# Kernel tuning notes

Hardware: AMD Instinct MI355X
Metric: run time of the kernel (lower is better)

## Reference

```python
import jax, jax.numpy as jnp
import numpy as np

B, S, D = 4, 2048, 1024


def setup_inputs() -> dict:
    key = jax.random.key(0)
    kq, k1, k2, k3 = jax.random.split(key, 4)
    w_scale = 1.0 / np.sqrt(D)  # ~ glorot scale for square Dense
    q = jax.random.normal(kq, (B, S, D), dtype=jnp.float32)
    Wq = jax.random.normal(k1, (D, D), dtype=jnp.float32) * w_scale
    Wk = jax.random.normal(k2, (D, D), dtype=jnp.float32) * w_scale  # unused in self-attn path (bug in original)
    Wv = jax.random.normal(k3, (D, D), dtype=jnp.float32) * w_scale
    # causal mask: 1 = masked (future), matching tf.where(mask == 1, -1e9, scores)
    mask = jnp.triu(jnp.ones((S, S), dtype=jnp.int32), k=1)
    return {"q": q, "Wq": Wq, "Wk": Wk, "Wv": Wv, "mask": mask}


def reference(q, Wq, Wk, Wv, mask):
    # Self-attention path of the original: k=None, v=None.
    WQ = jnp.einsum('bsd,de->bse', q, Wq)
    # Faithful to the original code: dense_v is applied for BOTH K and V.
    WKV = jnp.einsum('bsd,de->bse', q, Wv)
    d_k = jnp.asarray(D, dtype=q.dtype)
    scores = jnp.einsum('bqd,bkd->bqk', WQ, WKV) / jnp.sqrt(d_k)  # [B,S,S]
    scores = jnp.where(mask == 1, jnp.asarray(-1e9, scores.dtype), scores)
    attn = jax.nn.softmax(scores, axis=-1)
    return jnp.einsum('bqk,bkd->bqd', attn, WKV)
```

## Files before the change

### kernel.cpp

```cpp
#include <hip/hip_runtime.h>


typedef unsigned short u16;
typedef short short8 __attribute__((ext_vector_type(8)));
typedef float floatx4 __attribute__((ext_vector_type(4)));

#define S_LEN 2048
#define D_DIM 1024
#define BK 64

__device__ inline u16 f2b(float f) {
  unsigned u = __float_as_uint(f);
  return (u16)((u + 0x7fffu + ((u >> 16) & 1u)) >> 16);
}

__device__ __forceinline__ void gload16(const u16* g, u16* l) {
  __builtin_amdgcn_global_load_lds(
      (const __attribute__((address_space(1))) void*)g,
      (__attribute__((address_space(3))) void*)l, 16, 0, 0);
}

__global__ __launch_bounds__(256)
void prep(const float* __restrict__ q, u16* __restrict__ qb16,
          const float* __restrict__ Wq, u16* __restrict__ Wqt,
          const float* __restrict__ Wv, u16* __restrict__ Wvt,
          float* __restrict__ rowsum) {
  int id = blockIdx.x, tid = threadIdx.x;
  if (id < 4096) {
    if (id < 4) {
      int o = id * 2048 + tid * 8;
      float4 zz = {0.f, 0.f, 0.f, 0.f};
      *(float4*)&rowsum[o] = zz;
      *(float4*)&rowsum[o + 4] = zz;
    }
    size_t idx = ((size_t)id * 256 + tid) * 8;
    float4 a0 = *(const float4*)&q[idx];
    float4 a1 = *(const float4*)&q[idx + 4];
    short8 v;
    v[0] = (short)f2b(a0.x); v[1] = (short)f2b(a0.y);
    v[2] = (short)f2b(a0.z); v[3] = (short)f2b(a0.w);
    v[4] = (short)f2b(a1.x); v[5] = (short)f2b(a1.y);
    v[6] = (short)f2b(a1.z); v[7] = (short)f2b(a1.w);
    *(short8*)&qb16[idx] = v;
    return;
  }
  __shared__ u16 tile[64][65];
  int id2 = id - 4096;
  int z = id2 >> 8;
  int idx4 = id2 & 255;
  int c0 = (idx4 & 15) * 64, r0 = (idx4 >> 4) * 64;
  const float* src = z ? Wv : Wq;
  u16* dst = z ? Wvt : Wqt;
  int tx = tid & 63, ty = tid >> 6;
#pragma unroll
  for (int i = 0; i < 16; ++i)
    tile[i * 4 + ty][tx] =
        f2b(src[(size_t)(r0 + i * 4 + ty) * 1024 + (c0 + tx)]);
  __syncthreads();
#pragma unroll
  for (int i = 0; i < 16; ++i)
    dst[(size_t)(c0 + i * 4 + ty) * 1024 + (r0 + tx)] = tile[tx][i * 4 + ty];
}

__global__ __launch_bounds__(512, 2)
void gemm_proj(const u16* __restrict__ A, const u16* __restrict__ B0,
               const u16* __restrict__ B1, u16* __restrict__ C0,
               u16* __restrict__ C1, u16* __restrict__ WKVt) {
  __shared__ __align__(16) u16 lds[65536];

  int id = blockIdx.x;
  int xcd = id & 7, i5 = id >> 3;
  int m_idx = xcd * 4 + (i5 & 3);
  int n_idx = i5 >> 2;
  int z = n_idx >> 2;
  int n0 = (n_idx & 3) * 256;
  int m0 = m_idx * 256;
  const u16* Bp = z ? B1 : B0;
  u16* Cp = z ? C1 : C0;

  int tid = threadIdx.x;
  int wv = tid >> 6, lane = tid & 63, quad = lane >> 4, l15 = lane & 15;
  int wm = wv >> 2, wn = wv & 3;

  int off_g[2];
#pragma unroll
  for (int l = 0; l < 2; ++l) {
    int chunk = (wv * 2 + l) * 64 + lane;
    int r = chunk >> 3, cs = chunk & 7;
    off_g[l] = r * 1024 + (cs ^ (r & 7)) * 8;
  }
  const u16* As0 = A + (size_t)m0 * 1024;
  const u16* As1 = A + (size_t)(m0 + 128) * 1024;
  const u16* Bs0 = Bp + (size_t)n0 * 1024;
  const u16* Bs1 = Bp + (size_t)(n0 + 128) * 1024;

#define PSTAGE(src, reg)                                                     \
  {                                                                          \
    _Pragma("unroll") for (int l = 0; l < 2; ++l)                            \
        gload16((src) + off_g[l], &lds[(reg) * 8192 + (wv * 2 + l) * 512]);  \
  }

  int aoff[2], boff[2];
#pragma unroll
  for (int kk = 0; kk < 2; ++kk) {
    int c = ((kk * 4 + quad) ^ (l15 & 7)) * 8;
    aoff[kk] = l15 * 64 + c;
    boff[kk] = ((wn & 1) * 64 + l15) * 64 + c;
  }
  const u16* A0p = &lds[(0 + wm) * 8192];
  const u16* A1p = &lds[(4 + wm) * 8192];
  const u16* B0p = &lds[(2 + (wn >> 1)) * 8192];
  const u16* B1p = &lds[(6 + (wn >> 1)) * 8192];

  floatx4 acc[8][4];
#pragma unroll
  for (int i = 0; i < 8; ++i)
#pragma unroll
    for (int j = 0; j < 4; ++j) acc[i][j] = (floatx4){0.f, 0.f, 0.f, 0.f};

#define BARp() __builtin_amdgcn_s_barrier()
#define WLG() asm volatile("s_waitcnt lgkmcnt(0)" ::: "memory")
#define WVM(n) asm volatile("s_waitcnt vmcnt(" #n ")" ::: "memory")

#define RDA(dst, base, fb)                                                 \
  _Pragma("unroll") for (int f = 0; f < 4; ++f)                            \
  _Pragma("unroll") for (int kk = 0; kk < 2; ++kk)                         \
      dst[f][kk] = *(const short8*)&(base)[((fb) + f) * 1024 + aoff[kk]];
#define RDB(dst, base, fb)                                                 \
  _Pragma("unroll") for (int f = 0; f < 2; ++f)                            \
  _Pragma("unroll") for (int kk = 0; kk < 2; ++kk)                         \
      dst[f][kk] = *(const short8*)&(base)[((fb) + f) * 1024 + boff[kk]];
#define MMQ(mh, nh, afq, bfq)                                              \
  __builtin_amdgcn_s_setprio(1);                                           \
  _Pragma("unroll") for (int f = 0; f < 4; ++f)                            \
  _Pragma("unroll") for (int g2 = 0; g2 < 2; ++g2)                         \
  _Pragma("unroll") for (int kk = 0; kk < 2; ++kk)                         \
      acc[(mh) * 4 + f][(nh) * 2 + g2] =                                   \
          __builtin_amdgcn_mfma_f32_16x16x32_bf16(                         \
              afq[f][kk], bfq[g2][kk], acc[(mh) * 4 + f][(nh) * 2 + g2],   \
              0, 0, 0);                                                    \
  __builtin_amdgcn_s_setprio(0);

  PSTAGE(As0, 0); PSTAGE(As1, 1); PSTAGE(Bs0, 2); PSTAGE(Bs1, 3);
  PSTAGE(As0 + 64, 4); PSTAGE(As1 + 64, 5); PSTAGE(Bs0 + 64, 6);
  PSTAGE(Bs1 + 64, 7);
  WVM(8);
  BARp();

#pragma unroll 1
  for (int it = 0; it < 8; ++it) {
    int kb2 = it * 128 + 128, kb3 = it * 128 + 192;
    short8 af[4][2], bf0[2][2], bf1[2][2];
    RDA(af, A0p, 0); RDB(bf0, B0p, 0);
    BARp(); WLG();
    MMQ(0, 0, af, bf0);
    BARp();
    RDB(bf1, B0p, 2);
    BARp(); WLG();
    MMQ(0, 1, af, bf1);
    BARp();
    RDA(af, A0p, 4);
    if (it < 7) PSTAGE(Bs0 + kb2, 2);
    BARp(); WLG();
    MMQ(1, 1, af, bf1);
    BARp();
    if (it < 7) { PSTAGE(Bs1 + kb2, 3); PSTAGE(As0 + kb2, 0); }
    BARp();
    MMQ(1, 0, af, bf0);
    if (it < 7) { WVM(6); } else { WVM(0); }
    BARp();
    RDA(af, A1p, 0); RDB(bf0, B1p, 0);
    if (it < 7) PSTAGE(As1 + kb2, 1);
    BARp(); WLG();
    MMQ(0, 0, af, bf0);
    BARp();
    RDB(bf1, B1p, 2);
    BARp(); WLG();
    MMQ(0, 1, af, bf1);
    BARp();
    RDA(af, A1p, 4);
    if (it < 7) PSTAGE(Bs0 + kb3, 6);
    BARp(); WLG();
    MMQ(1, 1, af, bf1);
    BARp();
    if (it < 7) {
      PSTAGE(Bs1 + kb3, 7); PSTAGE(As0 + kb3, 4); PSTAGE(As1 + kb3, 5);
    }
    BARp();
    MMQ(1, 0, af, bf0);
    if (it < 7) WVM(8);
    BARp();
  }

  asm volatile("s_waitcnt vmcnt(0) lgkmcnt(0)" ::: "memory");
#pragma unroll
  for (int mf = 0; mf < 8; ++mf)
#pragma unroll
    for (int nf = 0; nf < 4; ++nf)
#pragma unroll
      for (int r = 0; r < 4; ++r)
        Cp[(size_t)(m0 + wm * 128 + mf * 16 + quad * 4 + r) * D_DIM +
           (n0 + wn * 64 + nf * 16 + l15)] = f2b(acc[mf][nf][r]);

  if (z) {
    int b = m0 >> 11, srow = m0 & 2047;
    u16* Wt = WKVt + (size_t)b * D_DIM * S_LEN;
#pragma unroll
    for (int ph = 0; ph < 2; ++ph) {
      BARp();
      if ((wn >> 1) == ph) {
#pragma unroll
        for (int mf = 0; mf < 8; ++mf)
#pragma unroll
          for (int nf = 0; nf < 4; ++nf)
#pragma unroll
            for (int r = 0; r < 4; ++r)
              lds[((wn & 1) * 64 + nf * 16 + l15) * 272 +
                  (wm * 128 + mf * 16 + quad * 4 + r)] = f2b(acc[mf][nf][r]);
      }
      BARp();
#pragma unroll
      for (int rr = 0; rr < 8; ++rr) {
        int idx = rr * 512 + tid;
        int dl = idx >> 5, sc = idx & 31;
        *(short8*)&Wt[(size_t)(n0 + ph * 128 + dl) * S_LEN + srow + sc * 8] =
            *(const short8*)&lds[dl * 272 + sc * 8];
      }
    }
  }
}

#define GEMM64_PROLOG()                                                       \
  __shared__ __align__(16) u16 Als[2][64 * BK];                               \
  __shared__ __align__(16) u16 Bls[2][128 * BK];                              \
  int tid = threadIdx.x;                                                      \
  int wave = tid >> 6, lane = tid & 63, quad = lane >> 4, l15 = lane & 15;    \
  int wr = (wave >> 1) * 32, wc = (wave & 1) * 64;                            \
  int arow = lane >> 3;                                                       \
  int acol = ((lane & 7) ^ (arow & 7)) << 3;                                  \
  floatx4 acc[2][4];                                                          \
  _Pragma("unroll") for (int i = 0; i < 2; ++i)                               \
  _Pragma("unroll") for (int j = 0; j < 4; ++j)                               \
      acc[i][j] = (floatx4){0.f, 0.f, 0.f, 0.f};

#define GEMM64_STAGE(buf, Aptr, lda, Bptr, ldb, kb)                           \
  {                                                                           \
    _Pragma("unroll") for (int p = 0; p < 2; ++p) {                           \
      int r0 = wave * 16 + p * 8;                                             \
      gload16(&(Aptr)[(size_t)(m0 + r0 + arow) * (lda) + (kb) + acol],        \
              &Als[buf][r0 * BK]);                                            \
    }                                                                         \
    _Pragma("unroll") for (int p = 0; p < 4; ++p) {                           \
      int r0 = wave * 32 + p * 8;                                             \
      gload16(&(Bptr)[(size_t)(n0 + r0 + arow) * (ldb) + (kb) + acol],        \
              &Bls[buf][r0 * BK]);                                            \
    }                                                                         \
  }

#define GEMM64_COMP(buf)                                                      \
  {                                                                           \
    const u16* Ab = &Als[buf][0];                                             \
    const u16* Bb = &Bls[buf][0];                                             \
    _Pragma("unroll") for (int kk8 = 0; kk8 < 8; kk8 += 4) {                  \
      int cg = (((kk8 + quad) & 7) ^ (l15 & 7)) << 3;                         \
      short8 af[2], bfr[4];                                                   \
      _Pragma("unroll") for (int i = 0; i < 2; ++i)                           \
          af[i] = *(const short8*)&Ab[(wr + i * 16 + l15) * BK + cg];         \
      _Pragma("unroll") for (int j = 0; j < 4; ++j)                           \
          bfr[j] = *(const short8*)&Bb[(wc + j * 16 + l15) * BK + cg];        \
      _Pragma("unroll") for (int i = 0; i < 2; ++i)                           \
      _Pragma("unroll") for (int j = 0; j < 4; ++j)                           \
          acc[i][j] = __builtin_amdgcn_mfma_f32_16x16x32_bf16(                \
              af[i], bfr[j], acc[i][j], 0, 0, 0);                             \
    }                                                                         \
  }

#define GEMM64_KLOOP(Aptr, lda, Bptr, ldb, KEND)                              \
  _Pragma("unroll 1") for (int kb = 0; kb < (KEND); kb += 2 * BK) {           \
    bool two = (kb + BK < (KEND));                                            \
    __syncthreads();                                                          \
    GEMM64_STAGE(0, Aptr, lda, Bptr, ldb, kb);                                \
    if (two) GEMM64_STAGE(1, Aptr, lda, Bptr, ldb, kb + BK);                  \
    __syncthreads();                                                          \
    GEMM64_COMP(0);                                                           \
    if (two) GEMM64_COMP(1);                                                  \
  }

__global__ __launch_bounds__(256)
void gemm_scores(const u16* __restrict__ WQ, const u16* __restrict__ WKV,
                 u16* __restrict__ Pp, float* __restrict__ rowsum) {
  int id = blockIdx.x;
  int xcd = id & 7;
  int b = xcd & 3, h = xcd >> 2;
  int t = id >> 3;
  int m = (int)((sqrtf(8.f * (float)t + 1.f) - 1.f) * 0.5f);
  while ((m + 1) * (m + 2) / 2 <= t) ++m;
  while (m * (m + 1) / 2 > t) --m;
  int bj = t - m * (m + 1) / 2;
  int bi = 2 * m + h;
  int m0 = bi * 64, n0 = bj * 128;
  const u16* A = WQ + (size_t)b * S_LEN * D_DIM;
  const u16* Bp = WKV + (size_t)b * S_LEN * D_DIM;
  GEMM64_PROLOG();
  GEMM64_KLOOP(A, D_DIM, Bp, D_DIM, D_DIM);
  u16* Pb = Pp + (size_t)b * S_LEN * S_LEN;
  float part[2][4];
#pragma unroll
  for (int i = 0; i < 2; ++i)
#pragma unroll
    for (int r = 0; r < 4; ++r) part[i][r] = 0.f;
#pragma unroll
  for (int i = 0; i < 2; ++i)
#pragma unroll
    for (int j = 0; j < 4; ++j) {
      int col = n0 + wc + j * 16 + l15;
#pragma unroll
      for (int r = 0; r < 4; ++r) {
        int row = m0 + wr + i * 16 + quad * 4 + r;
        float p = (col > row) ? 0.f : __expf(acc[i][j][r] * 0.03125f);
        Pb[(size_t)row * S_LEN + col] = f2b(p);
        part[i][r] += p;
      }
    }
#pragma unroll
  for (int i = 0; i < 2; ++i)
#pragma unroll
    for (int r = 0; r < 4; ++r) {
      float v = part[i][r];
#pragma unroll
      for (int off = 1; off < 16; off <<= 1) v += __shfl_xor(v, off, 64);
      part[i][r] = v;
    }
  if (l15 == 0) {
#pragma unroll
    for (int i = 0; i < 2; ++i)
#pragma unroll
      for (int r = 0; r < 4; ++r)
        atomicAdd(&rowsum[b * S_LEN + m0 + wr + i * 16 + quad * 4 + r],
                  part[i][r]);
  }
}

__global__ __launch_bounds__(256)
void gemm_pv(const u16* __restrict__ Pp, const u16* __restrict__ WKVt,
             const float* __restrict__ rowsum, float* __restrict__ out) {
  int id = blockIdx.x;
  int xcd = id & 7;
  int b = xcd & 3, h = xcd >> 2;
  int r_ = id >> 3;
  int mh = 15 - (r_ >> 3);
  int bi = 2 * mh + h;
  int bj = r_ & 7;
  int m0 = bi * 64, n0 = bj * 128;
  int kend = (bi + 1) * 64;
  const u16* A = Pp + (size_t)b * S_LEN * S_LEN;
  const u16* Bp = WKVt + (size_t)b * (size_t)D_DIM * S_LEN;
  GEMM64_PROLOG();
  GEMM64_KLOOP(A, S_LEN, Bp, S_LEN, kend);
  const float* rs = rowsum + b * S_LEN;
  float* Co = out + (size_t)b * S_LEN * D_DIM;
#pragma unroll
  for (int i = 0; i < 2; ++i)
#pragma unroll
    for (int r = 0; r < 4; ++r) {
      int row = m0 + wr + i * 16 + quad * 4 + r;
      float inv = 1.0f / rs[row];
#pragma unroll
      for (int j = 0; j < 4; ++j)
        Co[(size_t)row * D_DIM + (n0 + wc + j * 16 + l15)] =
            acc[i][j][r] * inv;
    }
}

extern "C" void kernel_launch(void* const* d_in, const int* in_sizes, int n_in,
                              void* d_out, int out_size, void* d_ws, size_t ws_size,
                              hipStream_t stream) {
  const float* q = (const float*)d_in[0];
  const float* Wq = (const float*)d_in[1];
  const float* Wv = (const float*)d_in[3];
  char* ws = (char*)d_ws;
  const size_t MB = 1024 * 1024;
  u16* Wqt = (u16*)(ws);
  u16* Wvt = (u16*)(ws + 2 * MB);
  u16* qb16 = (u16*)(ws + 4 * MB);
  u16* Pp = (u16*)(ws);
  u16* WQ = (u16*)(ws + 32 * MB);
  u16* WKV = (u16*)(ws + 48 * MB);
  u16* WKVt = (u16*)(ws + 64 * MB);
  float* rowsum = (float*)(ws + 80 * MB);

  prep<<<4608, 256, 0, stream>>>(q, qb16, Wq, Wqt, Wv, Wvt, rowsum);
  gemm_proj<<<256, 512, 0, stream>>>(qb16, Wqt, Wvt, WQ, WKV, WKVt);
  gemm_scores<<<1088, 256, 0, stream>>>(WQ, WKV, Pp, rowsum);
  gemm_pv<<<1024, 256, 0, stream>>>(Pp, WKVt, rowsum, (float*)d_out);
}
```

Before: 200.7 us.

## Fuse scores and PV GEMMs into persistent kernel with dependency-tracked work queue

Replaces the separate scores and PV kernels with one persistent kernel of 768 blocks that pull work items from a global atomic counter. Score tiles are issued first, in reverse order. Each PV tile spins until every score tile for its row block has finished and signalled through per-row-block done counters. The aim is to overlap the PV phase with the tail of the scores phase and remove the kernel boundary between them. The cost is spin-waiting, extra fences and atomics, and the risk of stalls if dependencies resolve late.

After: 522.5 us. 160% more time.

```diff
diff --git a/kernel.cpp b/kernel.cpp
--- a/kernel.cpp
+++ b/kernel.cpp
@@ -24,7 +24,7 @@
 void prep(const float* __restrict__ q, u16* __restrict__ qb16,
           const float* __restrict__ Wq, u16* __restrict__ Wqt,
           const float* __restrict__ Wv, u16* __restrict__ Wvt,
-          float* __restrict__ rowsum) {
+          float* __restrict__ rowsum, unsigned* __restrict__ ctl) {
   int id = blockIdx.x, tid = threadIdx.x;
   if (id < 4096) {
     if (id < 4) {
@@ -33,6 +33,7 @@
       *(float4*)&rowsum[o] = zz;
       *(float4*)&rowsum[o + 4] = zz;
     }
+    if (id == 4 && tid < 160) ctl[tid] = 0;
     size_t idx = ((size_t)id * 256 + tid) * 8;
     float4 a0 = *(const float4*)&q[idx];
     float4 a1 = *(const float4*)&q[idx + 4];
@@ -230,19 +231,6 @@
   }
 }
 
-#define GEMM64_PROLOG()                                                       \
-  __shared__ __align__(16) u16 Als[2][64 * BK];                               \
-  __shared__ __align__(16) u16 Bls[2][128 * BK];                              \
-  int tid = threadIdx.x;                                                      \
-  int wave = tid >> 6, lane = tid & 63, quad = lane >> 4, l15 = lane & 15;    \
-  int wr = (wave >> 1) * 32, wc = (wave & 1) * 64;                            \
-  int arow = lane >> 3;                                                       \
-  int acol = ((lane & 7) ^ (arow & 7)) << 3;                                  \
-  floatx4 acc[2][4];                                                          \
-  _Pragma("unroll") for (int i = 0; i < 2; ++i)                               \
-  _Pragma("unroll") for (int j = 0; j < 4; ++j)                               \
-      acc[i][j] = (floatx4){0.f, 0.f, 0.f, 0.f};
-
 #define GEMM64_STAGE(buf, Aptr, lda, Bptr, ldb, kb)                           \
   {                                                                           \
     _Pragma("unroll") for (int p = 0; p < 2; ++p) {                           \
@@ -287,89 +275,122 @@
   }
 
 __global__ __launch_bounds__(256)
-void gemm_scores(const u16* __restrict__ WQ, const u16* __restrict__ WKV,
-                 u16* __restrict__ Pp, float* __restrict__ rowsum) {
-  int id = blockIdx.x;
-  int xcd = id & 7;
-  int b = xcd & 3, h = xcd >> 2;
-  int t = id >> 3;
-  int m = (int)((sqrtf(8.f * (float)t + 1.f) - 1.f) * 0.5f);
-  while ((m + 1) * (m + 2) / 2 <= t) ++m;
-  while (m * (m + 1) / 2 > t) --m;
-  int bj = t - m * (m + 1) / 2;
-  int bi = 2 * m + h;
-  int m0 = bi * 64, n0 = bj * 128;
-  const u16* A = WQ + (size_t)b * S_LEN * D_DIM;
-  const u16* Bp = WKV + (size_t)b * S_LEN * D_DIM;
-  GEMM64_PROLOG();
-  GEMM64_KLOOP(A, D_DIM, Bp, D_DIM, D_DIM);
-  u16* Pb = Pp + (size_t)b * S_LEN * S_LEN;
-  float part[2][4];
-#pragma unroll
-  for (int i = 0; i < 2; ++i)
-#pragma unroll
-    for (int r = 0; r < 4; ++r) part[i][r] = 0.f;
-#pragma unroll
-  for (int i = 0; i < 2; ++i)
-#pragma unroll
-    for (int j = 0; j < 4; ++j) {
-      int col = n0 + wc + j * 16 + l15;
-#pragma unroll
-      for (int r = 0; r < 4; ++r) {
-        int row = m0 + wr + i * 16 + quad * 4 + r;
-        float p = (col > row) ? 0.f : __expf(acc[i][j][r] * 0.03125f);
-        Pb[(size_t)row * S_LEN + col] = f2b(p);
-        part[i][r] += p;
+void gemm_sp(const u16* __restrict__ WQ, const u16* __restrict__ WKV,
+             const u16* __restrict__ WKVt, u16* __restrict__ Pp,
+             float* __restrict__ rowsum, unsigned* __restrict__ ctl,
+             float* __restrict__ out) {
+  __shared__ __align__(16) u16 Als[2][64 * BK];
+  __shared__ __align__(16) u16 Bls[2][128 * BK];
+  __shared__ int s_item;
+  int tid = threadIdx.x;
+  int wave = tid >> 6, lane = tid & 63, quad = lane >> 4, l15 = lane & 15;
+  int wr = (wave >> 1) * 32, wc = (wave & 1) * 64;
+  int arow = lane >> 3;
+  int acol = ((lane & 7) ^ (arow & 7)) << 3;
+  unsigned* qctr = ctl;
+  unsigned* done = ctl + 32;
+
+  for (;;) {
+    __syncthreads();
+    if (tid == 0) s_item = (int)atomicAdd(qctr, 1u);
+    __syncthreads();
+    int item = s_item;
+    if (item >= 2112) break;
+
+    floatx4 acc[2][4];
+#pragma unroll
+    for (int i = 0; i < 2; ++i)
+#pragma unroll
+      for (int j = 0; j < 4; ++j) acc[i][j] = (floatx4){0.f, 0.f, 0.f, 0.f};
+
+    if (item < 1088) {
+      int oid = 1087 - item;
+      int xcd = oid & 7;
+      int b = xcd & 3, h = xcd >> 2;
+      int t = oid >> 3;
+      int m = (int)((sqrtf(8.f * (float)t + 1.f) - 1.f) * 0.5f);
+      while ((m + 1) * (m + 2) / 2 <= t) ++m;
+      while (m * (m + 1) / 2 > t) --m;
+      int bj = t - m * (m + 1) / 2;
+      int bi = 2 * m + h;
+      int m0 = bi * 64, n0 = bj * 128;
+      const u16* A = WQ + (size_t)b * S_LEN * D_DIM;
+      const u16* Bp = WKV + (size_t)b * S_LEN * D_DIM;
+      GEMM64_KLOOP(A, D_DIM, Bp, D_DIM, D_DIM);
+      u16* Pb = Pp + (size_t)b * S_LEN * S_LEN;
+      float part[2][4];
+#pragma unroll
+      for (int i = 0; i < 2; ++i)
+#pragma unroll
+        for (int r = 0; r < 4; ++r) part[i][r] = 0.f;
+#pragma unroll
+      for (int i = 0; i < 2; ++i)
+#pragma unroll
+        for (int j = 0; j < 4; ++j) {
+          int col = n0 + wc + j * 16 + l15;
+#pragma unroll
+          for (int r = 0; r < 4; ++r) {
+            int row = m0 + wr + i * 16 + quad * 4 + r;
+            float p = (col > row) ? 0.f : __expf(acc[i][j][r] * 0.03125f);
+            Pb[(size_t)row * S_LEN + col] = f2b(p);
+            part[i][r] += p;
+          }
+        }
+#pragma unroll
+      for (int i = 0; i < 2; ++i)
+#pragma unroll
+        for (int r = 0; r < 4; ++r) {
+          float v = part[i][r];
+#pragma unroll
+          for (int off = 1; off < 16; off <<= 1) v += __shfl_xor(v, off, 64);
+          part[i][r] = v;
+        }
+      if (l15 == 0) {
+#pragma unroll
+        for (int i = 0; i < 2; ++i)
+#pragma unroll
+          for (int r = 0; r < 4; ++r)
+            atomicAdd(&rowsum[b * S_LEN + m0 + wr + i * 16 + quad * 4 + r],
+                      part[i][r]);
       }
+      __threadfence();
+      __syncthreads();
+      if (tid == 0) atomicAdd(&done[b * 32 + bi], 1u);
+    } else {
+      int p_ = item - 1088;
+      int xcd = p_ & 7;
+      int b = xcd & 3, h = xcd >> 2;
+      int r_ = p_ >> 3;
+      int mh = 15 - (r_ >> 3);
+      int bi = 2 * mh + h;
+      int bj = r_ & 7;
+      int m0 = bi * 64, n0 = bj * 128;
+      int kend = (bi + 1) * 64;
+      unsigned need = (unsigned)((bi >> 1) + 1);
+      if (tid == 0) {
+        volatile unsigned* dv = &done[b * 32 + bi];
+        while (*dv < need) __builtin_amdgcn_s_sleep(16);
+      }
+      __syncthreads();
+      __threadfence();
+      const u16* A = Pp + (size_t)b * S_LEN * S_LEN;
+      const u16* Bp = WKVt + (size_t)b * (size_t)D_DIM * S_LEN;
+      GEMM64_KLOOP(A, S_LEN, Bp, S_LEN, kend);
+      const float* rs = rowsum + b * S_LEN;
+      float* Co = out + (size_t)b * S_LEN * D_DIM;
+#pragma unroll
+      for (int i = 0; i < 2; ++i)
+#pragma unroll
+        for (int r = 0; r < 4; ++r) {
+          int row = m0 + wr + i * 16 + quad * 4 + r;
+          float inv = 1.0f / rs[row];
+#pragma unroll
+          for (int j = 0; j < 4; ++j)
+            Co[(size_t)row * D_DIM + (n0 + wc + j * 16 + l15)] =
+                acc[i][j][r] * inv;
+        }
     }
-#pragma unroll
-  for (int i = 0; i < 2; ++i)
-#pragma unroll
-    for (int r = 0; r < 4; ++r) {
-      float v = part[i][r];
-#pragma unroll
-      for (int off = 1; off < 16; off <<= 1) v += __shfl_xor(v, off, 64);
-      part[i][r] = v;
-    }
-  if (l15 == 0) {
-#pragma unroll
-    for (int i = 0; i < 2; ++i)
-#pragma unroll
-      for (int r = 0; r < 4; ++r)
-        atomicAdd(&rowsum[b * S_LEN + m0 + wr + i * 16 + quad * 4 + r],
-                  part[i][r]);
-  }
-}
-
-__global__ __launch_bounds__(256)
-void gemm_pv(const u16* __restrict__ Pp, const u16* __restrict__ WKVt,
-             const float* __restrict__ rowsum, float* __restrict__ out) {
-  int id = blockIdx.x;
-  int xcd = id & 7;
-  int b = xcd & 3, h = xcd >> 2;
-  int r_ = id >> 3;
-  int mh = 15 - (r_ >> 3);
-  int bi = 2 * mh + h;
-  int bj = r_ & 7;
-  int m0 = bi * 64, n0 = bj * 128;
-  int kend = (bi + 1) * 64;
-  const u16* A = Pp + (size_t)b * S_LEN * S_LEN;
-  const u16* Bp = WKVt + (size_t)b * (size_t)D_DIM * S_LEN;
-  GEMM64_PROLOG();
-  GEMM64_KLOOP(A, S_LEN, Bp, S_LEN, kend);
-  const float* rs = rowsum + b * S_LEN;
-  float* Co = out + (size_t)b * S_LEN * D_DIM;
-#pragma unroll
-  for (int i = 0; i < 2; ++i)
-#pragma unroll
-    for (int r = 0; r < 4; ++r) {
-      int row = m0 + wr + i * 16 + quad * 4 + r;
-      float inv = 1.0f / rs[row];
-#pragma unroll
-      for (int j = 0; j < 4; ++j)
-        Co[(size_t)row * D_DIM + (n0 + wc + j * 16 + l15)] =
-            acc[i][j][r] * inv;
-    }
+  }
 }
 
 extern "C" void kernel_launch(void* const* d_in, const int* in_sizes, int n_in,
@@ -388,9 +409,10 @@
   u16* WKV = (u16*)(ws + 48 * MB);
   u16* WKVt = (u16*)(ws + 64 * MB);
   float* rowsum = (float*)(ws + 80 * MB);
-
-  prep<<<4608, 256, 0, stream>>>(q, qb16, Wq, Wqt, Wv, Wvt, rowsum);
+  unsigned* ctl = (unsigned*)(ws + 80 * MB + 32 * 1024);
+
+  prep<<<4608, 256, 0, stream>>>(q, qb16, Wq, Wqt, Wv, Wvt, rowsum, ctl);
   gemm_proj<<<256, 512, 0, stream>>>(qb16, Wqt, Wvt, WQ, WKV, WKVt);
-  gemm_scores<<<1088, 256, 0, stream>>>(WQ, WKV, Pp, rowsum);
-  gemm_pv<<<1024, 256, 0, stream>>>(Pp, WKVt, rowsum, (float*)d_out);
-}
+  gemm_sp<<<768, 256, 0, stream>>>(WQ, WKV, WKVt, Pp, rowsum, ctl,
+                                   (float*)d_out);
+}
```

## Merge scores and PV kernels into one persistent cooperative kernel with grid sync

Applied to the files above, without the earlier changes.

Combines the scores and PV GEMM stages into a single persistent cooperative kernel of 768 blocks. Each block walks the scores tiles, waits at a grid-wide barrier, then walks the PV tiles. The goal is to save one kernel launch and the tail gap between the two stages. In exchange, occupancy is capped at 3 blocks per CU by the launch bounds, the tiles are statically strided so load balance across blocks can be poor, and a grid sync is added. If the cooperative launch fails, the code falls back to the original two launches.

Result: slower. 470.2 us (+134.3%).

```diff
diff --git a/kernel.cpp b/kernel.cpp
--- a/kernel.cpp
+++ b/kernel.cpp
@@ -1,4 +1,5 @@
 #include <hip/hip_runtime.h>
+#include <hip/hip_cooperative_groups.h>
 
 
 typedef unsigned short u16;
@@ -286,90 +287,117 @@
     if (two) GEMM64_COMP(1);                                                  \
   }
 
+#define SCORES_TILE(id_)                                                      \
+  {                                                                           \
+    int xcd = (id_) & 7;                                                      \
+    int b = xcd & 3, h = xcd >> 2;                                            \
+    int t = (id_) >> 3;                                                       \
+    int m = (int)((sqrtf(8.f * (float)t + 1.f) - 1.f) * 0.5f);                \
+    while ((m + 1) * (m + 2) / 2 <= t) ++m;                                   \
+    while (m * (m + 1) / 2 > t) --m;                                          \
+    int bj = t - m * (m + 1) / 2;                                             \
+    int bi = 2 * m + h;                                                       \
+    int m0 = bi * 64, n0 = bj * 128;                                          \
+    const u16* A = WQ + (size_t)b * S_LEN * D_DIM;                            \
+    const u16* Bp = WKV + (size_t)b * S_LEN * D_DIM;                          \
+    floatx4 acc[2][4];                                                        \
+    _Pragma("unroll") for (int i = 0; i < 2; ++i)                             \
+    _Pragma("unroll") for (int j = 0; j < 4; ++j)                             \
+        acc[i][j] = (floatx4){0.f, 0.f, 0.f, 0.f};                            \
+    GEMM64_KLOOP(A, D_DIM, Bp, D_DIM, D_DIM);                                 \
+    u16* Pb = Pp + (size_t)b * S_LEN * S_LEN;                                 \
+    float part[2][4];                                                         \
+    _Pragma("unroll") for (int i = 0; i < 2; ++i)                             \
+    _Pragma("unroll") for (int r = 0; r < 4; ++r) part[i][r] = 0.f;           \
+    _Pragma("unroll") for (int i = 0; i < 2; ++i)                             \
+    _Pragma("unroll") for (int j = 0; j < 4; ++j) {                           \
+      int col = n0 + wc + j * 16 + l15;                                       \
+      _Pragma("unroll") for (int r = 0; r < 4; ++r) {                         \
+        int row = m0 + wr + i * 16 + quad * 4 + r;                            \
+        float p = (col > row) ? 0.f : __expf(acc[i][j][r] * 0.03125f);        \
+        Pb[(size_t)row * S_LEN + col] = f2b(p);                               \
+        part[i][r] += p;                                                      \
+      }                                                                       \
+    }                                                                         \
+    _Pragma("unroll") for (int i = 0; i < 2; ++i)                             \
+    _Pragma("unroll") for (int r = 0; r < 4; ++r) {                           \
+      float v = part[i][r];                                                   \
+      _Pragma("unroll") for (int off = 1; off < 16; off <<= 1)                \
+          v += __shfl_xor(v, off, 64);                                        \
+      part[i][r] = v;                                                         \
+    }                                                                         \
+    if (l15 == 0) {                                                           \
+      _Pragma("unroll") for (int i = 0; i < 2; ++i)                           \
+      _Pragma("unroll") for (int r = 0; r < 4; ++r)                           \
+          atomicAdd(&rowsum[b * S_LEN + m0 + wr + i * 16 + quad * 4 + r],     \
+                    part[i][r]);                                              \
+    }                                                                         \
+  }
+
+#define PV_TILE(id_)                                                          \
+  {                                                                           \
+    int xcd = (id_) & 7;                                                      \
+    int b = xcd & 3, h = xcd >> 2;                                            \
+    int r_ = (id_) >> 3;                                                      \
+    int mh = 15 - (r_ >> 3);                                                  \
+    int bi = 2 * mh + h;                                                      \
+    int bj = r_ & 7;                                                          \
+    int m0 = bi * 64, n0 = bj * 128;                                          \
+    int kend = (bi + 1) * 64;                                                 \
+    const u16* A = Pp + (size_t)b * S_LEN * S_LEN;                            \
+    const u16* Bp = WKVt + (size_t)b * (size_t)D_DIM * S_LEN;                 \
+    floatx4 acc[2][4];                                                        \
+    _Pragma("unroll") for (int i = 0; i < 2; ++i)                             \
+    _Pragma("unroll") for (int j = 0; j < 4; ++j)                             \
+        acc[i][j] = (floatx4){0.f, 0.f, 0.f, 0.f};                            \
+    GEMM64_KLOOP(A, S_LEN, Bp, S_LEN, kend);                                  \
+    const float* rs = rowsum + b * S_LEN;                                     \
+    float* Co = out + (size_t)b * S_LEN * D_DIM;                              \
+    _Pragma("unroll") for (int i = 0; i < 2; ++i)                             \
+    _Pragma("unroll") for (int r = 0; r < 4; ++r) {                           \
+      int row = m0 + wr + i * 16 + quad * 4 + r;                              \
+      float inv = 1.0f / rs[row];                                             \
+      _Pragma("unroll") for (int j = 0; j < 4; ++j)                           \
+          Co[(size_t)row * D_DIM + (n0 + wc + j * 16 + l15)] =                \
+              acc[i][j][r] * inv;                                             \
+    }                                                                         \
+  }
+
 __global__ __launch_bounds__(256)
 void gemm_scores(const u16* __restrict__ WQ, const u16* __restrict__ WKV,
                  u16* __restrict__ Pp, float* __restrict__ rowsum) {
-  int id = blockIdx.x;
-  int xcd = id & 7;
-  int b = xcd & 3, h = xcd >> 2;
-  int t = id >> 3;
-  int m = (int)((sqrtf(8.f * (float)t + 1.f) - 1.f) * 0.5f);
-  while ((m + 1) * (m + 2) / 2 <= t) ++m;
-  while (m * (m + 1) / 2 > t) --m;
-  int bj = t - m * (m + 1) / 2;
-  int bi = 2 * m + h;
-  int m0 = bi * 64, n0 = bj * 128;
-  const u16* A = WQ + (size_t)b * S_LEN * D_DIM;
-  const u16* Bp = WKV + (size_t)b * S_LEN * D_DIM;
   GEMM64_PROLOG();
-  GEMM64_KLOOP(A, D_DIM, Bp, D_DIM, D_DIM);
-  u16* Pb = Pp + (size_t)b * S_LEN * S_LEN;
-  float part[2][4];
-#pragma unroll
-  for (int i = 0; i < 2; ++i)
-#pragma unroll
-    for (int r = 0; r < 4; ++r) part[i][r] = 0.f;
-#pragma unroll
-  for (int i = 0; i < 2; ++i)
-#pragma unroll
-    for (int j = 0; j < 4; ++j) {
-      int col = n0 + wc + j * 16 + l15;
-#pragma unroll
-      for (int r = 0; r < 4; ++r) {
-        int row = m0 + wr + i * 16 + quad * 4 + r;
-        float p = (col > row) ? 0.f : __expf(acc[i][j][r] * 0.03125f);
-        Pb[(size_t)row * S_LEN + col] = f2b(p);
-        part[i][r] += p;
-      }
-    }
-#pragma unroll
-  for (int i = 0; i < 2; ++i)
-#pragma unroll
-    for (int r = 0; r < 4; ++r) {
-      float v = part[i][r];
-#pragma unroll
-      for (int off = 1; off < 16; off <<= 1) v += __shfl_xor(v, off, 64);
-      part[i][r] = v;
-    }
-  if (l15 == 0) {
-#pragma unroll
-    for (int i = 0; i < 2; ++i)
-#pragma unroll
-      for (int r = 0; r < 4; ++r)
-        atomicAdd(&rowsum[b * S_LEN + m0 + wr + i * 16 + quad * 4 + r],
-                  part[i][r]);
-  }
+  SCORES_TILE(blockIdx.x);
 }
 
 __global__ __launch_bounds__(256)
 void gemm_pv(const u16* __restrict__ Pp, const u16* __restrict__ WKVt,
              const float* __restrict__ rowsum, float* __restrict__ out) {
-  int id = blockIdx.x;
-  int xcd = id & 7;
-  int b = xcd & 3, h = xcd >> 2;
-  int r_ = id >> 3;
-  int mh = 15 - (r_ >> 3);
-  int bi = 2 * mh + h;
-  int bj = r_ & 7;
-  int m0 = bi * 64, n0 = bj * 128;
-  int kend = (bi + 1) * 64;
-  const u16* A = Pp + (size_t)b * S_LEN * S_LEN;
-  const u16* Bp = WKVt + (size_t)b * (size_t)D_DIM * S_LEN;
   GEMM64_PROLOG();
-  GEMM64_KLOOP(A, S_LEN, Bp, S_LEN, kend);
-  const float* rs = rowsum + b * S_LEN;
-  float* Co = out + (size_t)b * S_LEN * D_DIM;
-#pragma unroll
-  for (int i = 0; i < 2; ++i)
-#pragma unroll
-    for (int r = 0; r < 4; ++r) {
-      int row = m0 + wr + i * 16 + quad * 4 + r;
-      float inv = 1.0f / rs[row];
-#pragma unroll
-      for (int j = 0; j < 4; ++j)
-        Co[(size_t)row * D_DIM + (n0 + wc + j * 16 + l15)] =
-            acc[i][j][r] * inv;
-    }
+  PV_TILE(blockIdx.x);
+}
+
+__global__ __launch_bounds__(256, 3)
+void gemm_sp(const u16* __restrict__ WQ, const u16* __restrict__ WKV,
+             const u16* __restrict__ WKVt, u16* __restrict__ Pp,
+             float* __restrict__ rowsum, float* __restrict__ out) {
+  GEMM64_PROLOG();
+  (void)acc;
+#pragma unroll 1
+  for (int s = 0; s < 2; ++s) {
+    int id = (int)blockIdx.x + s * 768;
+    if (id >= 1088) break;
+    SCORES_TILE(id);
+  }
+  __threadfence();
+  cooperative_groups::this_grid().sync();
+  __threadfence();
+#pragma unroll 1
+  for (int s = 0; s < 2; ++s) {
+    int id = (int)blockIdx.x + s * 768;
+    if (id >= 1024) break;
+    PV_TILE(id);
+  }
 }
 
 extern "C" void kernel_launch(void* const* d_in, const int* in_sizes, int n_in,
@@ -388,9 +416,20 @@
   u16* WKV = (u16*)(ws + 48 * MB);
   u16* WKVt = (u16*)(ws + 64 * MB);
   float* rowsum = (float*)(ws + 80 * MB);
+  float* outp = (float*)d_out;
 
   prep<<<4608, 256, 0, stream>>>(q, qb16, Wq, Wqt, Wv, Wvt, rowsum);
   gemm_proj<<<256, 512, 0, stream>>>(qb16, Wqt, Wvt, WQ, WKV, WKVt);
-  gemm_scores<<<1088, 256, 0, stream>>>(WQ, WKV, Pp, rowsum);
-  gemm_pv<<<1024, 256, 0, stream>>>(Pp, WKVt, rowsum, (float*)d_out);
-}
+
+  const u16* cWQ = WQ;
+  const u16* cWKV = WKV;
+  const u16* cWKVt = WKVt;
+  void* args[] = {(void*)&cWQ, (void*)&cWKV, (void*)&cWKVt,
+                  (void*)&Pp,  (void*)&rowsum, (void*)&outp};
+  hipError_t e = hipLaunchCooperativeKernel((const void*)gemm_sp, dim3(768),
+                                            dim3(256), args, 0, stream);
+  if (e != hipSuccess) {
+    gemm_scores<<<1088, 256, 0, stream>>>(WQ, WKV, Pp, rowsum);
+    gemm_pv<<<1024, 256, 0, stream>>>(Pp, WKVt, rowsum, outp);
+  }
+}
```
